# Kernel tuning notes

Measured on AMD Instinct MI355X. Metric: run time of the kernel, lower is better.

The kernel has to match this reference:

```python
import jax, jax.numpy as jnp
import numpy as np

N = 50000      # nodes
E = 400000     # edges (avg degree 8)
F_IN = 128     # input feature dim
H = 4          # heads (layer 1)
D = 128        # hidden per head
C = 3          # classes (layer 2 out, 1 head)
EPS = 1e-5     # BatchNorm eps
SLOPE = 0.2    # LeakyReLU negative slope (DGL GATConv default)


def setup_inputs() -> dict:
    key = jax.random.key(0)
    ks = jax.random.split(key, 16)
    s = jnp.float32(0.05)
    return {
        "features": jax.random.normal(ks[0], (N, F_IN), jnp.float32),
        "src": jax.random.randint(ks[1], (E,), 0, N, jnp.int32),
        "dst": jax.random.randint(ks[2], (E,), 0, N, jnp.int32),
        # GATConv layer 1 params
        "W1": jax.random.normal(ks[3], (F_IN, H * D), jnp.float32) * s,
        "al1": jax.random.normal(ks[4], (H, D), jnp.float32) * s,
        "ar1": jax.random.normal(ks[5], (H, D), jnp.float32) * s,
        "b1": jnp.zeros((H * D,), jnp.float32),
        "Wres1": jax.random.normal(ks[6], (F_IN, H * D), jnp.float32) * s,
        # BatchNorm1d (inference mode)
        "bn_gamma": jnp.ones((H * D,), jnp.float32),
        "bn_beta": jnp.zeros((H * D,), jnp.float32),
        "bn_mean": jnp.zeros((H * D,), jnp.float32),
        "bn_var": jnp.ones((H * D,), jnp.float32),
        # GATConv layer 2 params (1 head, C out)
        "W2": jax.random.normal(ks[7], (H * D, C), jnp.float32) * s,
        "al2": jax.random.normal(ks[8], (1, C), jnp.float32) * s,
        "ar2": jax.random.normal(ks[9], (1, C), jnp.float32) * s,
        "b2": jnp.zeros((C,), jnp.float32),
        "Wres2": jax.random.normal(ks[10], (H * D, C), jnp.float32) * s,
    }


def _gat_layer(x, src, dst, W, attn_l, attn_r, bias, Wres, heads, dim):
    """DGL GATConv (eval mode): gather, LeakyReLU score, segment softmax,
    weighted scatter-sum, linear residual, bias."""
    n = x.shape[0]
    z = (x @ W).reshape(n, heads, dim)                 # [N,H,D]
    el = jnp.sum(z * attn_l, axis=-1)                  # [N,H]
    er = jnp.sum(z * attn_r, axis=-1)                  # [N,H]
    e = jax.nn.leaky_relu(el[src] + er[dst], SLOPE)    # [E,H]
    # segment softmax over incoming edges of each dst node
    m = jax.ops.segment_max(e, dst, num_segments=n)    # [N,H]
    ex = jnp.exp(e - m[dst])                           # [E,H]
    den = jax.ops.segment_sum(ex, dst, num_segments=n) # [N,H]
    alpha = ex / den[dst]                              # [E,H]
    # weighted message aggregation
    rst = jax.ops.segment_sum(z[src] * alpha[..., None], dst, num_segments=n)  # [N,H,D]
    res = (x @ Wres).reshape(n, heads, dim)
    return rst + res + bias.reshape(1, heads, dim)


def reference(features, src, dst, W1, al1, ar1, b1, Wres1,
              bn_gamma, bn_beta, bn_mean, bn_var,
              W2, al2, ar2, b2, Wres2):
    h = _gat_layer(features, src, dst, W1, al1, ar1, b1, Wres1, H, D)
    h = h.reshape(N, H * D)
    # BatchNorm1d (inference) + ELU; dropout is identity in eval mode
    h = (h - bn_mean) * jax.lax.rsqrt(bn_var + EPS) * bn_gamma + bn_beta
    h = jax.nn.elu(h)
    h = _gat_layer(h, src, dst, W2, al2, ar2, b2, Wres2, 1, C)
    return h[:, 0, :]  # squeeze head dim -> [N, C]
```

## Files before the change

### kernel.cpp

```cpp
#include <hip/hip_runtime.h>
#include <hip/hip_bf16.h>

#define N_NODES 50000
#define N_EDGES 400000
#define FIN     128
#define HD      512
#define SLOPE   0.2f
#define NB_X    782

typedef __hip_bfloat16 bf16;
typedef __bf16 bf16x8 __attribute__((ext_vector_type(8)));
typedef __bf16 bf16x4 __attribute__((ext_vector_type(4)));
typedef __bf16 bf16x2 __attribute__((ext_vector_type(2)));
typedef float  f32x4  __attribute__((ext_vector_type(4)));
typedef float  f32x2  __attribute__((ext_vector_type(2)));

__global__ void sentinel_k(float* out, int n) {
    int i = blockIdx.x * 256 + threadIdx.x;
    if (i < n) out[i] = 12288.0f;
}

__global__ __launch_bounds__(256) void prep_k(const float* __restrict__ W1, const float* __restrict__ Wres1,
                                              const float* __restrict__ al1, const float* __restrict__ ar1,
                                              const float* __restrict__ W2, const float* __restrict__ Wres2,
                                              const float* __restrict__ b1,
                                              const float* __restrict__ bnm, const float* __restrict__ bnv,
                                              const float* __restrict__ bng, const float* __restrict__ bnb,
                                              bf16* __restrict__ Wfrag, float* __restrict__ tab,
                                              bf16* __restrict__ wlrb,
                                              int* __restrict__ deg) {
    int b = blockIdx.x;
    if (b < 196) {
        int i = b * 256 + threadIdx.x;
        if (i < N_NODES) deg[i] = 0;
        return;
    }
    b -= 196;
    if (b < 64) {
        int f = b * 256 + threadIdx.x;
        int lane = f & 63, unit = f >> 6;
        int tile = unit >> 3, ks = unit & 7;
        int cl = lane & 15, rg = lane >> 4;
        int gc = tile * 16 + cl;
        int k0 = ks * 32 + rg * 8;
        bf16x8 v;
#pragma unroll
        for (int j = 0; j < 8; ++j) {
            int kk = k0 + j;
            float x = (kk < 128) ? W1[kk * HD + gc] : Wres1[(kk - 128) * HD + gc];
            v[j] = (__bf16)x;
        }
        *reinterpret_cast<bf16x8*>(reinterpret_cast<char*>(Wfrag) + (size_t)f * 16) = v;
        return;
    }
    b -= 64;
    if (b < 16) {
        int i = b * 256 + threadIdx.x;
        int gc = i >> 3, c = i & 7;
        float v;
        if (c < 2) {
            float rs = rsqrtf(bnv[gc] + 1e-5f) * bng[gc];
            v = (c == 0) ? rs : (b1[gc] - bnm[gc]) * rs + bnb[gc];
        } else if (c < 5) {
            v = W2[gc * 3 + (c - 2)];
        } else {
            v = Wres2[gc * 3 + (c - 5)];
        }
        tab[i] = v;
        return;
    }
    for (int i = 0; i < 8; ++i) {
        int e = i * 256 + threadIdx.x;
        int ks = e >> 9, lane = (e >> 3) & 63, j = e & 7;
        int r = lane & 15, rg = lane >> 4;
        int k = ks * 32 + rg * 8 + j;
        float v = 0.f;
        if (r < 4) {
            for (int d = 0; d < 128; ++d) v += W1[k * HD + r * 128 + d] * al1[r * 128 + d];
        } else if (r < 8) {
            int h = r - 4;
            for (int d = 0; d < 128; ++d) v += W1[k * HD + h * 128 + d] * ar1[h * 128 + d];
        }
        wlrb[e] = __float2bfloat16(v);
    }
}

__global__ __launch_bounds__(256) void eler_k(const float* __restrict__ X,
                                              const bf16* __restrict__ wlrb,
                                              float* __restrict__ el, float* __restrict__ er,
                                              bf16* __restrict__ Xb,
                                              const int* __restrict__ dst, int* __restrict__ deg) {
    if (blockIdx.x >= NB_X) {
        int e = (blockIdx.x - NB_X) * 256 + threadIdx.x;
        if (e < N_EDGES) atomicAdd(&deg[dst[e]], 1);
        return;
    }
    __shared__ __align__(16) char XSb[64 * 256];
    const int t = threadIdx.x;
    const int w = t >> 6, lane = t & 63;
    const int cl = lane & 15, rg = lane >> 4;
    const int m0 = blockIdx.x * 64;

#pragma unroll
    for (int j = 0; j < 8; ++j) {
        int e = j * 1024 + t * 4;
        int row = e >> 7, col = e & 127;
        int grow = m0 + row;
        int gc = grow < N_NODES ? grow : N_NODES - 1;
        f32x4 v = *reinterpret_cast<const f32x4*>(X + (size_t)gc * FIN + col);
        bf16x4 bv = {(__bf16)v[0], (__bf16)v[1], (__bf16)v[2], (__bf16)v[3]};
        if (grow < N_NODES)
            *reinterpret_cast<bf16x4*>(Xb + (size_t)grow * FIN + col) = bv;
        int byte = (row * 256 + col * 2) ^ ((row & 7) << 4);
        *reinterpret_cast<bf16x4*>(XSb + byte) = bv;
    }
    __syncthreads();

    f32x4 a = {0.f, 0.f, 0.f, 0.f};
    const int row = w * 16 + cl;
    const int swz = (row & 7) << 4;
#pragma unroll
    for (int ks = 0; ks < 4; ++ks) {
        bf16x8 af = *reinterpret_cast<const bf16x8*>(
            reinterpret_cast<const char*>(wlrb) + ((size_t)(ks * 64 + lane)) * 16);
        int byte = (row * 256 + ks * 64 + rg * 16) ^ swz;
        bf16x8 bf = *reinterpret_cast<const bf16x8*>(XSb + byte);
        a = __builtin_amdgcn_mfma_f32_16x16x32_bf16(af, bf, a, 0, 0, 0);
    }
    int n = m0 + row;
    if (n < N_NODES) {
        if (rg == 0)      *reinterpret_cast<float4*>(el + (size_t)n * 4) = make_float4(a[0], a[1], a[2], a[3]);
        else if (rg == 1) *reinterpret_cast<float4*>(er + (size_t)n * 4) = make_float4(a[0], a[1], a[2], a[3]);
    }
}

__global__ __launch_bounds__(256) void scan1_k(const int* __restrict__ deg,
                                               int* __restrict__ rowptr, int* __restrict__ blksum) {
    __shared__ int wsum[4];
    int t = threadIdx.x, b = blockIdx.x;
    int i = b * 256 + t;
    int v = (i < N_NODES) ? deg[i] : 0;
    int lane = t & 63, w = t >> 6;
    int x = v;
#pragma unroll
    for (int off = 1; off < 64; off <<= 1) {
        int y = __shfl_up(x, off);
        if (lane >= off) x += y;
    }
    if (lane == 63) wsum[w] = x;
    __syncthreads();
    int wadd = 0;
    if (w > 0) wadd += wsum[0];
    if (w > 1) wadd += wsum[1];
    if (w > 2) wadd += wsum[2];
    int incl = x + wadd;
    if (i < N_NODES) rowptr[i] = incl - v;
    if (t == 255) blksum[b] = incl;
}

__global__ __launch_bounds__(256) void scan2_k(int* __restrict__ blksum) {
    __shared__ int wsum[4];
    int t = threadIdx.x;
    int v = (t < 196) ? blksum[t] : 0;
    int lane = t & 63, w = t >> 6;
    int x = v;
#pragma unroll
    for (int off = 1; off < 64; off <<= 1) {
        int y = __shfl_up(x, off);
        if (lane >= off) x += y;
    }
    if (lane == 63) wsum[w] = x;
    __syncthreads();
    int wadd = 0;
    if (w > 0) wadd += wsum[0];
    if (w > 1) wadd += wsum[1];
    if (w > 2) wadd += wsum[2];
    if (t < 196) blksum[t] = x + wadd - v;
}

__global__ __launch_bounds__(256) void scan3_k(const int* __restrict__ blksum,
                                               int* __restrict__ rowptr, int* __restrict__ cursor) {
    int b = blockIdx.x;
    int i = b * 256 + threadIdx.x;
    if (i < N_NODES) {
        int v = rowptr[i] + blksum[b];
        rowptr[i] = v;
        cursor[i] = v;
    }
    if (i == 0) rowptr[N_NODES] = N_EDGES;
}

__global__ void fill_k(const int* __restrict__ src, const int* __restrict__ dst,
                       int* __restrict__ cursor, int* __restrict__ csr) {
    int e = blockIdx.x * 256 + threadIdx.x;
    if (e < N_EDGES) {
        int pos = atomicAdd(&cursor[dst[e]], 1);
        csr[pos] = src[e];
    }
}

__global__ __launch_bounds__(1024) void aggX_k(const int* __restrict__ rowptr, const int* __restrict__ csr,
                                               const float* __restrict__ el, const float* __restrict__ er,
                                               const bf16* __restrict__ Xb, bf16* __restrict__ AGGb) {
    __shared__ int    ssrc[16][64];
    __shared__ float4 spe4[16][64];

    const int w = threadIdx.x >> 6, lane = threadIdx.x & 63;
    const int n = blockIdx.x * 16 + w;
    const int beg = rowptr[n];
    const int deg = rowptr[n + 1] - beg;
    const float4 ern = *reinterpret_cast<const float4*>(er + (size_t)n * 4);
    const char* Xbc = reinterpret_cast<const char*>(Xb);

    f32x2 acc[4] = {{0.f,0.f},{0.f,0.f},{0.f,0.f},{0.f,0.f}};
    float4 den = make_float4(0.f, 0.f, 0.f, 0.f);

    for (int base = 0; base < deg; base += 64) {
        const int cnt = min(64, deg - base);
        if (lane < cnt) {
            int s = csr[beg + base + lane];
            ssrc[w][lane] = s;
            float4 e4 = *reinterpret_cast<const float4*>(el + (size_t)s * 4);
            float4 p; float e;
            e = e4.x + ern.x; e = e > 0.f ? e : SLOPE * e; p.x = __expf(e);
            e = e4.y + ern.y; e = e > 0.f ? e : SLOPE * e; p.y = __expf(e);
            e = e4.z + ern.z; e = e > 0.f ? e : SLOPE * e; p.z = __expf(e);
            e = e4.w + ern.w; e = e > 0.f ? e : SLOPE * e; p.w = __expf(e);
            den.x += p.x; den.y += p.y; den.z += p.z; den.w += p.w;
            spe4[w][lane] = p;
        }
        asm volatile("s_waitcnt lgkmcnt(0)" ::: "memory");
        for (int jj = 0; jj < cnt; jj += 4) {
            unsigned xv[4]; float4 pk[4];
#pragma unroll
            for (int k2 = 0; k2 < 4; ++k2) {
                int j2 = jj + k2;
                int jc = j2 < cnt ? j2 : cnt - 1;
                int s = ssrc[w][jc];
                xv[k2] = *reinterpret_cast<const unsigned*>(Xbc + (size_t)s * 256 + lane * 4);
                float4 p = spe4[w][jc];
                if (j2 >= cnt) p = make_float4(0.f, 0.f, 0.f, 0.f);
                pk[k2] = p;
            }
#pragma unroll
            for (int k2 = 0; k2 < 4; ++k2) {
                f32x2 x2 = {__uint_as_float(xv[k2] << 16), __uint_as_float(xv[k2] & 0xffff0000u)};
                acc[0] += pk[k2].x * x2;
                acc[1] += pk[k2].y * x2;
                acc[2] += pk[k2].z * x2;
                acc[3] += pk[k2].w * x2;
            }
        }
        asm volatile("s_waitcnt lgkmcnt(0)" ::: "memory");
    }

#pragma unroll
    for (int off = 32; off > 0; off >>= 1) {
        den.x += __shfl_xor(den.x, off);
        den.y += __shfl_xor(den.y, off);
        den.z += __shfl_xor(den.z, off);
        den.w += __shfl_xor(den.w, off);
    }
    float inv[4] = {0.f, 0.f, 0.f, 0.f};
    if (deg > 0) {
        inv[0] = 1.f / den.x; inv[1] = 1.f / den.y;
        inv[2] = 1.f / den.z; inv[3] = 1.f / den.w;
    }
#pragma unroll
    for (int h = 0; h < 4; ++h) {
        bf16x2 v = {(__bf16)(acc[h][0] * inv[h]), (__bf16)(acc[h][1] * inv[h])};
        *reinterpret_cast<bf16x2*>(AGGb + (size_t)n * 512 + h * 128 + lane * 2) = v;
    }
}

__global__ __launch_bounds__(256) void gemm2_k(
    const bf16* __restrict__ Xb, const bf16* __restrict__ AGGb,
    const bf16* __restrict__ Wfrag, const float* __restrict__ tab,
    const float* __restrict__ al2, const float* __restrict__ ar2,
    float* __restrict__ node2) {
    __shared__ __align__(16) char XS[32 * 256];
    __shared__ __align__(16) char AGS[32 * 1024];
    __shared__ float zsum[4][32][6];

    const int t = threadIdx.x;
    const int w = t >> 6, lane = t & 63;
    const int cl = lane & 15, rg = lane >> 4;
    const int m0 = blockIdx.x * 32;

#pragma unroll
    for (int j = 0; j < 2; ++j) {
        int L = j * 4096 + t * 16;
        int row = L >> 8, col = L & 255;
        int grow = m0 + row; grow = grow < N_NODES ? grow : N_NODES - 1;
        bf16x8 v = *reinterpret_cast<const bf16x8*>(
            reinterpret_cast<const char*>(Xb) + (size_t)grow * 256 + col);
        int byte = (row * 256 + col) ^ ((row & 7) << 4);
        *reinterpret_cast<bf16x8*>(XS + byte) = v;
    }
#pragma unroll
    for (int j = 0; j < 8; ++j) {
        int L = j * 4096 + t * 16;
        int row = L >> 10, col = L & 1023;
        int grow = m0 + row; grow = grow < N_NODES ? grow : N_NODES - 1;
        bf16x8 v = *reinterpret_cast<const bf16x8*>(
            reinterpret_cast<const char*>(AGGb) + (size_t)grow * 1024 + col);
        int byte = (row * 1024 + col) ^ ((row & 7) << 4);
        *reinterpret_cast<bf16x8*>(AGS + byte) = v;
    }
    __syncthreads();

    float z2p[2][3] = {}, r2p[2][3] = {};

#pragma unroll
    for (int ct = 0; ct < 8; ++ct) {
        const int unit = (w * 8 + ct) * 8;
        bf16x8 af[8];
#pragma unroll
        for (int ks = 0; ks < 8; ++ks)
            af[ks] = *reinterpret_cast<const bf16x8*>(
                reinterpret_cast<const char*>(Wfrag) + ((size_t)(unit + ks) * 64 + lane) * 16);
        const int gcl = w * 128 + ct * 16 + rg * 4;
        f32x4 t0[4], t1[4];
#pragma unroll
        for (int i = 0; i < 4; ++i) {
            t0[i] = *reinterpret_cast<const f32x4*>(tab + (size_t)(gcl + i) * 8);
            t1[i] = *reinterpret_cast<const f32x4*>(tab + (size_t)(gcl + i) * 8 + 4);
        }
#pragma unroll
        for (int mt = 0; mt < 2; ++mt) {
            int row = mt * 16 + cl;
            int swz = (row & 7) << 4;
            f32x4 a = {0.f, 0.f, 0.f, 0.f};
#pragma unroll
            for (int ks = 0; ks < 4; ++ks) {
                int byte = (row * 1024 + w * 256 + ks * 64 + rg * 16) ^ swz;
                bf16x8 bfr = *reinterpret_cast<const bf16x8*>(AGS + byte);
                a = __builtin_amdgcn_mfma_f32_16x16x32_bf16(af[ks], bfr, a, 0, 0, 0);
            }
#pragma unroll
            for (int ks = 0; ks < 4; ++ks) {
                int byte = (row * 256 + ks * 64 + rg * 16) ^ swz;
                bf16x8 bfr = *reinterpret_cast<const bf16x8*>(XS + byte);
                a = __builtin_amdgcn_mfma_f32_16x16x32_bf16(af[ks + 4], bfr, a, 0, 0, 0);
            }
#pragma unroll
            for (int i = 0; i < 4; ++i) {
                float hv = a[i] * t0[i][0] + t0[i][1];
                hv = hv > 0.f ? hv : (__expf(hv) - 1.f);
                z2p[mt][0] += hv * t0[i][2]; z2p[mt][1] += hv * t0[i][3]; z2p[mt][2] += hv * t1[i][0];
                r2p[mt][0] += hv * t1[i][1]; r2p[mt][1] += hv * t1[i][2]; r2p[mt][2] += hv * t1[i][3];
            }
        }
    }

#pragma unroll
    for (int mt = 0; mt < 2; ++mt)
#pragma unroll
        for (int c = 0; c < 3; ++c) {
            z2p[mt][c] += __shfl_xor(z2p[mt][c], 16);
            z2p[mt][c] += __shfl_xor(z2p[mt][c], 32);
            r2p[mt][c] += __shfl_xor(r2p[mt][c], 16);
            r2p[mt][c] += __shfl_xor(r2p[mt][c], 32);
        }
    if (rg == 0) {
#pragma unroll
        for (int mt = 0; mt < 2; ++mt) {
            int nl = mt * 16 + cl;
            zsum[w][nl][0] = z2p[mt][0]; zsum[w][nl][1] = z2p[mt][1]; zsum[w][nl][2] = z2p[mt][2];
            zsum[w][nl][3] = r2p[mt][0]; zsum[w][nl][4] = r2p[mt][1]; zsum[w][nl][5] = r2p[mt][2];
        }
    }
    __syncthreads();
    if (t < 32) {
        float v[6];
#pragma unroll
        for (int c = 0; c < 6; ++c)
            v[c] = zsum[0][t][c] + zsum[1][t][c] + zsum[2][t][c] + zsum[3][t][c];
        int n = m0 + t;
        if (n < N_NODES) {
            float e2l = v[0] * al2[0] + v[1] * al2[1] + v[2] * al2[2];
            float e2r = v[0] * ar2[0] + v[1] * ar2[1] + v[2] * ar2[2];
            *reinterpret_cast<float4*>(node2 + (size_t)n * 8) = make_float4(v[0], v[1], v[2], e2l);
            *reinterpret_cast<float4*>(node2 + (size_t)n * 8 + 4) = make_float4(v[3], v[4], v[5], e2r);
        }
    }
}

__global__ __launch_bounds__(256) void agg2_k(const int* __restrict__ rowptr, const int* __restrict__ csr,
                                              const float* __restrict__ node2,
                                              const float* __restrict__ b2, float* __restrict__ out) {
    int wv = threadIdx.x >> 6, lane = threadIdx.x & 63;
    int n = blockIdx.x * 4 + wv;
    int beg = rowptr[n], deg = rowptr[n + 1] - beg;
    float ern = node2[(size_t)n * 8 + 7];
    float den = 0.f, a0 = 0.f, a1 = 0.f, a2 = 0.f;
    for (int j = lane; j < deg; j += 64) {
        int s = csr[beg + j];
        float4 v = *reinterpret_cast<const float4*>(node2 + (size_t)s * 8);
        float e = v.w + ern;
        e = e > 0.f ? e : SLOPE * e;
        float p = __expf(e);
        den += p;
        a0 += p * v.x; a1 += p * v.y; a2 += p * v.z;
    }
#pragma unroll
    for (int off = 32; off > 0; off >>= 1) {
        den += __shfl_xor(den, off);
        a0 += __shfl_xor(a0, off); a1 += __shfl_xor(a1, off); a2 += __shfl_xor(a2, off);
    }
    if (lane == 0) {
        float inv = deg > 0 ? 1.f / den : 0.f;
        float4 r = *reinterpret_cast<const float4*>(node2 + (size_t)n * 8 + 4);
        out[(size_t)n * 3 + 0] = a0 * inv + r.x + b2[0];
        out[(size_t)n * 3 + 1] = a1 * inv + r.y + b2[1];
        out[(size_t)n * 3 + 2] = a2 * inv + r.z + b2[2];
    }
}

extern "C" void kernel_launch(void* const* d_in, const int* in_sizes, int n_in,
                              void* d_out, int out_size, void* d_ws, size_t ws_size,
                              hipStream_t stream) {
    const float* X     = (const float*)d_in[0];
    const int*   src   = (const int*)d_in[1];
    const int*   dst   = (const int*)d_in[2];
    const float* W1    = (const float*)d_in[3];
    const float* al1   = (const float*)d_in[4];
    const float* ar1   = (const float*)d_in[5];
    const float* b1    = (const float*)d_in[6];
    const float* Wres1 = (const float*)d_in[7];
    const float* bng   = (const float*)d_in[8];
    const float* bnb   = (const float*)d_in[9];
    const float* bnm   = (const float*)d_in[10];
    const float* bnv   = (const float*)d_in[11];
    const float* W2    = (const float*)d_in[12];
    const float* al2   = (const float*)d_in[13];
    const float* ar2   = (const float*)d_in[14];
    const float* b2    = (const float*)d_in[15];
    const float* Wres2 = (const float*)d_in[16];
    float* out = (float*)d_out;

    char* p = (char*)d_ws;
    auto carve = [&](size_t bytes) -> char* {
        char* r = p;
        p += (bytes + 255) & ~(size_t)255;
        return r;
    };
    bf16*  Wfrag  = (bf16*)carve((size_t)512 * 256 * 2);
    float* tab    = (float*)carve((size_t)512 * 8 * 4);
    bf16*  wlrb   = (bf16*)carve((size_t)2048 * 2);
    float* el     = (float*)carve((size_t)N_NODES * 4 * 4);
    float* er     = (float*)carve((size_t)N_NODES * 4 * 4);
    int*   deg    = (int*)carve((size_t)N_NODES * 4);
    int*   rowptr = (int*)carve((size_t)(N_NODES + 1) * 4);
    int*   cursor = (int*)carve((size_t)N_NODES * 4);
    int*   blksum = (int*)carve((size_t)256 * 4);
    int*   csr    = (int*)carve((size_t)N_EDGES * 4);
    bf16*  Xb     = (bf16*)carve((size_t)N_NODES * FIN * 2);
    bf16*  AGGb   = (bf16*)carve((size_t)N_NODES * 512 * 2);
    float* node2  = (float*)carve((size_t)N_NODES * 8 * 4);
    size_t need = (size_t)(p - (char*)d_ws);
    if (need > ws_size) {
        sentinel_k<<<(out_size + 255) / 256, 256, 0, stream>>>(out, out_size);
        return;
    }

    prep_k<<<196 + 64 + 16 + 1, 256, 0, stream>>>(W1, Wres1, al1, ar1, W2, Wres2, b1,
                                                  bnm, bnv, bng, bnb, Wfrag, tab, wlrb, deg);
    eler_k<<<NB_X + (N_EDGES + 255) / 256, 256, 0, stream>>>(X, wlrb, el, er, Xb, dst, deg);
    scan1_k<<<196, 256, 0, stream>>>(deg, rowptr, blksum);
    scan2_k<<<1, 256, 0, stream>>>(blksum);
    scan3_k<<<196, 256, 0, stream>>>(blksum, rowptr, cursor);
    fill_k<<<(N_EDGES + 255) / 256, 256, 0, stream>>>(src, dst, cursor, csr);
    aggX_k<<<N_NODES / 16, 1024, 0, stream>>>(rowptr, csr, el, er, Xb, AGGb);
    gemm2_k<<<(N_NODES + 31) / 32, 256, 0, stream>>>(Xb, AGGb, Wfrag, tab, al2, ar2, node2);
    agg2_k<<<N_NODES / 4, 256, 0, stream>>>(rowptr, csr, node2, b2, out);
}
```

Before: 180.4 us.

## Drop scan3 pass, split edges across half-waves, defer softmax normalisation to GEMM

Removes the third scan kernel: CSR offsets are now computed on the fly as a local prefix plus a block sum, with a separately zeroed slot counter, and the degree array is reused. The aggregation kernel now has each half-wave handle alternate edges with 8-byte feature loads, combined by a cross-half shuffle. The softmax denominator is no longer normalised there; it is written to a side buffer and applied inside the following GEMM as a per-row scale on a separate MFMA accumulator. The goal is one fewer launch, fewer cross-lane reductions and more memory-level parallelism in the gather, at the cost of an extra accumulator and a serial denominator sum done by four lanes.

```diff
diff --git a/kernel.cpp b/kernel.cpp
--- a/kernel.cpp
+++ b/kernel.cpp
@@ -28,11 +28,11 @@
                                               const float* __restrict__ bng, const float* __restrict__ bnb,
                                               bf16* __restrict__ Wfrag, float* __restrict__ tab,
                                               bf16* __restrict__ wlrb,
-                                              int* __restrict__ deg) {
+                                              int* __restrict__ deg, int* __restrict__ cur0) {
     int b = blockIdx.x;
     if (b < 196) {
         int i = b * 256 + threadIdx.x;
-        if (i < N_NODES) deg[i] = 0;
+        if (i < N_NODES) { deg[i] = 0; cur0[i] = 0; }
         return;
     }
     b -= 196;
@@ -135,7 +135,7 @@
 }
 
 __global__ __launch_bounds__(256) void scan1_k(const int* __restrict__ deg,
-                                               int* __restrict__ rowptr, int* __restrict__ blksum) {
+                                               int* __restrict__ rloc, int* __restrict__ blksum) {
     __shared__ int wsum[4];
     int t = threadIdx.x, b = blockIdx.x;
     int i = b * 256 + t;
@@ -154,7 +154,7 @@
     if (w > 1) wadd += wsum[1];
     if (w > 2) wadd += wsum[2];
     int incl = x + wadd;
-    if (i < N_NODES) rowptr[i] = incl - v;
+    if (i < N_NODES) rloc[i] = incl - v;
     if (t == 255) blksum[b] = incl;
 }
 
@@ -178,42 +178,36 @@
     if (t < 196) blksum[t] = x + wadd - v;
 }
 
-__global__ __launch_bounds__(256) void scan3_k(const int* __restrict__ blksum,
-                                               int* __restrict__ rowptr, int* __restrict__ cursor) {
-    int b = blockIdx.x;
-    int i = b * 256 + threadIdx.x;
-    if (i < N_NODES) {
-        int v = rowptr[i] + blksum[b];
-        rowptr[i] = v;
-        cursor[i] = v;
-    }
-    if (i == 0) rowptr[N_NODES] = N_EDGES;
-}
-
 __global__ void fill_k(const int* __restrict__ src, const int* __restrict__ dst,
-                       int* __restrict__ cursor, int* __restrict__ csr) {
+                       const int* __restrict__ rloc, const int* __restrict__ bsum,
+                       int* __restrict__ cur0, int* __restrict__ csr) {
     int e = blockIdx.x * 256 + threadIdx.x;
     if (e < N_EDGES) {
-        int pos = atomicAdd(&cursor[dst[e]], 1);
-        csr[pos] = src[e];
-    }
-}
-
-__global__ __launch_bounds__(1024) void aggX_k(const int* __restrict__ rowptr, const int* __restrict__ csr,
+        int d = dst[e];
+        int slot = atomicAdd(&cur0[d], 1);
+        csr[rloc[d] + bsum[d >> 8] + slot] = src[e];
+    }
+}
+
+__global__ __launch_bounds__(1024) void aggX_k(const int* __restrict__ rloc, const int* __restrict__ bsum,
+                                               const int* __restrict__ degA, const int* __restrict__ csr,
                                                const float* __restrict__ el, const float* __restrict__ er,
-                                               const bf16* __restrict__ Xb, bf16* __restrict__ AGGb) {
+                                               const bf16* __restrict__ Xb, bf16* __restrict__ AGGb,
+                                               float* __restrict__ den4) {
     __shared__ int    ssrc[16][64];
     __shared__ float4 spe4[16][64];
 
     const int w = threadIdx.x >> 6, lane = threadIdx.x & 63;
+    const int sub = lane >> 5, ll = lane & 31;
     const int n = blockIdx.x * 16 + w;
-    const int beg = rowptr[n];
-    const int deg = rowptr[n + 1] - beg;
+    const int beg = rloc[n] + bsum[n >> 8];
+    const int deg = degA[n];
     const float4 ern = *reinterpret_cast<const float4*>(er + (size_t)n * 4);
     const char* Xbc = reinterpret_cast<const char*>(Xb);
 
-    f32x2 acc[4] = {{0.f,0.f},{0.f,0.f},{0.f,0.f},{0.f,0.f}};
-    float4 den = make_float4(0.f, 0.f, 0.f, 0.f);
+    f32x2 accA[4] = {{0.f,0.f},{0.f,0.f},{0.f,0.f},{0.f,0.f}};
+    f32x2 accB[4] = {{0.f,0.f},{0.f,0.f},{0.f,0.f},{0.f,0.f}};
+    float dreg = 0.f;
 
     for (int base = 0; base < deg; base += 64) {
         const int cnt = min(64, deg - base);
@@ -226,55 +220,51 @@
             e = e4.y + ern.y; e = e > 0.f ? e : SLOPE * e; p.y = __expf(e);
             e = e4.z + ern.z; e = e > 0.f ? e : SLOPE * e; p.z = __expf(e);
             e = e4.w + ern.w; e = e > 0.f ? e : SLOPE * e; p.w = __expf(e);
-            den.x += p.x; den.y += p.y; den.z += p.z; den.w += p.w;
             spe4[w][lane] = p;
         }
         asm volatile("s_waitcnt lgkmcnt(0)" ::: "memory");
-        for (int jj = 0; jj < cnt; jj += 4) {
-            unsigned xv[4]; float4 pk[4];
-#pragma unroll
-            for (int k2 = 0; k2 < 4; ++k2) {
-                int j2 = jj + k2;
-                int jc = j2 < cnt ? j2 : cnt - 1;
-                int s = ssrc[w][jc];
-                xv[k2] = *reinterpret_cast<const unsigned*>(Xbc + (size_t)s * 256 + lane * 4);
-                float4 p = spe4[w][jc];
-                if (j2 >= cnt) p = make_float4(0.f, 0.f, 0.f, 0.f);
-                pk[k2] = p;
-            }
-#pragma unroll
-            for (int k2 = 0; k2 < 4; ++k2) {
-                f32x2 x2 = {__uint_as_float(xv[k2] << 16), __uint_as_float(xv[k2] & 0xffff0000u)};
-                acc[0] += pk[k2].x * x2;
-                acc[1] += pk[k2].y * x2;
-                acc[2] += pk[k2].z * x2;
-                acc[3] += pk[k2].w * x2;
-            }
+        if (lane < 4) {
+            for (int j = 0; j < cnt; ++j)
+                dreg += reinterpret_cast<const float*>(&spe4[w][j])[lane];
+        }
+        for (int jj = 0; jj < cnt; jj += 2) {
+            int j2 = jj + sub;
+            int jc = j2 < cnt ? j2 : cnt - 1;
+            int s = ssrc[w][jc];
+            uint2 xv = *reinterpret_cast<const uint2*>(Xbc + (size_t)s * 256 + ll * 8);
+            float4 p = spe4[w][jc];
+            if (j2 >= cnt) p = make_float4(0.f, 0.f, 0.f, 0.f);
+            f32x2 xlo = {__uint_as_float(xv.x << 16), __uint_as_float(xv.x & 0xffff0000u)};
+            f32x2 xhi = {__uint_as_float(xv.y << 16), __uint_as_float(xv.y & 0xffff0000u)};
+            accA[0] += p.x * xlo; accB[0] += p.x * xhi;
+            accA[1] += p.y * xlo; accB[1] += p.y * xhi;
+            accA[2] += p.z * xlo; accB[2] += p.z * xhi;
+            accA[3] += p.w * xlo; accB[3] += p.w * xhi;
         }
         asm volatile("s_waitcnt lgkmcnt(0)" ::: "memory");
     }
 
 #pragma unroll
-    for (int off = 32; off > 0; off >>= 1) {
-        den.x += __shfl_xor(den.x, off);
-        den.y += __shfl_xor(den.y, off);
-        den.z += __shfl_xor(den.z, off);
-        den.w += __shfl_xor(den.w, off);
-    }
-    float inv[4] = {0.f, 0.f, 0.f, 0.f};
-    if (deg > 0) {
-        inv[0] = 1.f / den.x; inv[1] = 1.f / den.y;
-        inv[2] = 1.f / den.z; inv[3] = 1.f / den.w;
-    }
-#pragma unroll
     for (int h = 0; h < 4; ++h) {
-        bf16x2 v = {(__bf16)(acc[h][0] * inv[h]), (__bf16)(acc[h][1] * inv[h])};
-        *reinterpret_cast<bf16x2*>(AGGb + (size_t)n * 512 + h * 128 + lane * 2) = v;
-    }
+        accA[h][0] += __shfl_xor(accA[h][0], 32);
+        accA[h][1] += __shfl_xor(accA[h][1], 32);
+        accB[h][0] += __shfl_xor(accB[h][0], 32);
+        accB[h][1] += __shfl_xor(accB[h][1], 32);
+    }
+    if (sub == 0) {
+#pragma unroll
+        for (int h = 0; h < 4; ++h) {
+            bf16x4 v = {(__bf16)accA[h][0], (__bf16)accA[h][1],
+                        (__bf16)accB[h][0], (__bf16)accB[h][1]};
+            *reinterpret_cast<bf16x4*>(AGGb + (size_t)n * 512 + h * 128 + ll * 4) = v;
+        }
+    }
+    if (lane < 4) den4[(size_t)n * 4 + lane] = dreg;
 }
 
 __global__ __launch_bounds__(256) void gemm2_k(
     const bf16* __restrict__ Xb, const bf16* __restrict__ AGGb,
+    const float* __restrict__ den4,
     const bf16* __restrict__ Wfrag, const float* __restrict__ tab,
     const float* __restrict__ al2, const float* __restrict__ ar2,
     float* __restrict__ node2) {
@@ -309,6 +299,15 @@
     }
     __syncthreads();
 
+    float invden[2];
+#pragma unroll
+    for (int mt = 0; mt < 2; ++mt) {
+        int nn = m0 + mt * 16 + cl;
+        nn = nn < N_NODES ? nn : N_NODES - 1;
+        float d = den4[(size_t)nn * 4 + w];
+        invden[mt] = d > 0.f ? 1.f / d : 0.f;
+    }
+
     float z2p[2][3] = {}, r2p[2][3] = {};
 
 #pragma unroll
@@ -330,22 +329,24 @@
         for (int mt = 0; mt < 2; ++mt) {
             int row = mt * 16 + cl;
             int swz = (row & 7) << 4;
-            f32x4 a = {0.f, 0.f, 0.f, 0.f};
+            f32x4 aA = {0.f, 0.f, 0.f, 0.f};
+            f32x4 aX = {0.f, 0.f, 0.f, 0.f};
 #pragma unroll
             for (int ks = 0; ks < 4; ++ks) {
                 int byte = (row * 1024 + w * 256 + ks * 64 + rg * 16) ^ swz;
                 bf16x8 bfr = *reinterpret_cast<const bf16x8*>(AGS + byte);
-                a = __builtin_amdgcn_mfma_f32_16x16x32_bf16(af[ks], bfr, a, 0, 0, 0);
+                aA = __builtin_amdgcn_mfma_f32_16x16x32_bf16(af[ks], bfr, aA, 0, 0, 0);
             }
 #pragma unroll
             for (int ks = 0; ks < 4; ++ks) {
                 int byte = (row * 256 + ks * 64 + rg * 16) ^ swz;
                 bf16x8 bfr = *reinterpret_cast<const bf16x8*>(XS + byte);
-                a = __builtin_amdgcn_mfma_f32_16x16x32_bf16(af[ks + 4], bfr, a, 0, 0, 0);
+                aX = __builtin_amdgcn_mfma_f32_16x16x32_bf16(af[ks + 4], bfr, aX, 0, 0, 0);
             }
 #pragma unroll
             for (int i = 0; i < 4; ++i) {
-                float hv = a[i] * t0[i][0] + t0[i][1];
+                float z = aA[i] * invden[mt] + aX[i];
+                float hv = z * t0[i][0] + t0[i][1];
                 hv = hv > 0.f ? hv : (__expf(hv) - 1.f);
                 z2p[mt][0] += hv * t0[i][2]; z2p[mt][1] += hv * t0[i][3]; z2p[mt][2] += hv * t1[i][0];
                 r2p[mt][0] += hv * t1[i][1]; r2p[mt][1] += hv * t1[i][2]; r2p[mt][2] += hv * t1[i][3];
@@ -386,12 +387,14 @@
     }
 }
 
-__global__ __launch_bounds__(256) void agg2_k(const int* __restrict__ rowptr, const int* __restrict__ csr,
+__global__ __launch_bounds__(256) void agg2_k(const int* __restrict__ rloc, const int* __restrict__ bsum,
+                                              const int* __restrict__ degA, const int* __restrict__ csr,
                                               const float* __restrict__ node2,
                                               const float* __restrict__ b2, float* __restrict__ out) {
     int wv = threadIdx.x >> 6, lane = threadIdx.x & 63;
     int n = blockIdx.x * 4 + wv;
-    int beg = rowptr[n], deg = rowptr[n + 1] - beg;
+    int beg = rloc[n] + bsum[n >> 8];
+    int deg = degA[n];
     float ern = node2[(size_t)n * 8 + 7];
     float den = 0.f, a0 = 0.f, a1 = 0.f, a2 = 0.f;
     for (int j = lane; j < deg; j += 64) {
@@ -451,12 +454,13 @@
     float* el     = (float*)carve((size_t)N_NODES * 4 * 4);
     float* er     = (float*)carve((size_t)N_NODES * 4 * 4);
     int*   deg    = (int*)carve((size_t)N_NODES * 4);
-    int*   rowptr = (int*)carve((size_t)(N_NODES + 1) * 4);
-    int*   cursor = (int*)carve((size_t)N_NODES * 4);
-    int*   blksum = (int*)carve((size_t)256 * 4);
+    int*   rloc   = (int*)carve((size_t)(N_NODES + 256) * 4);
+    int*   cur0   = (int*)carve((size_t)N_NODES * 4);
+    int*   bsum   = (int*)carve((size_t)256 * 4);
     int*   csr    = (int*)carve((size_t)N_EDGES * 4);
     bf16*  Xb     = (bf16*)carve((size_t)N_NODES * FIN * 2);
     bf16*  AGGb   = (bf16*)carve((size_t)N_NODES * 512 * 2);
+    float* den4   = (float*)carve((size_t)(N_NODES + 64) * 4 * 4);
     float* node2  = (float*)carve((size_t)N_NODES * 8 * 4);
     size_t need = (size_t)(p - (char*)d_ws);
     if (need > ws_size) {
@@ -465,13 +469,12 @@
     }
 
     prep_k<<<196 + 64 + 16 + 1, 256, 0, stream>>>(W1, Wres1, al1, ar1, W2, Wres2, b1,
-                                                  bnm, bnv, bng, bnb, Wfrag, tab, wlrb, deg);
+                                                  bnm, bnv, bng, bnb, Wfrag, tab, wlrb, deg, cur0);
     eler_k<<<NB_X + (N_EDGES + 255) / 256, 256, 0, stream>>>(X, wlrb, el, er, Xb, dst, deg);
-    scan1_k<<<196, 256, 0, stream>>>(deg, rowptr, blksum);
-    scan2_k<<<1, 256, 0, stream>>>(blksum);
-    scan3_k<<<196, 256, 0, stream>>>(blksum, rowptr, cursor);
-    fill_k<<<(N_EDGES + 255) / 256, 256, 0, stream>>>(src, dst, cursor, csr);
-    aggX_k<<<N_NODES / 16, 1024, 0, stream>>>(rowptr, csr, el, er, Xb, AGGb);
-    gemm2_k<<<(N_NODES + 31) / 32, 256, 0, stream>>>(Xb, AGGb, Wfrag, tab, al2, ar2, node2);
-    agg2_k<<<N_NODES / 4, 256, 0, stream>>>(rowptr, csr, node2, b2, out);
-}
+    scan1_k<<<196, 256, 0, stream>>>(deg, rloc, bsum);
+    scan2_k<<<1, 256, 0, stream>>>(bsum);
+    fill_k<<<(N_EDGES + 255) / 256, 256, 0, stream>>>(src, dst, rloc, bsum, cur0, csr);
+    aggX_k<<<N_NODES / 16, 1024, 0, stream>>>(rloc, bsum, deg, csr, el, er, Xb, AGGb, den4);
+    gemm2_k<<<(N_NODES + 31) / 32, 256, 0, stream>>>(Xb, AGGb, den4, Wfrag, tab, al2, ar2, node2);
+    agg2_k<<<N_NODES / 4, 256, 0, stream>>>(rloc, bsum, deg, csr, node2, b2, out);
+}
```

Result: no change. 183.6 us (+1.8%).
